# Kernel optimization log

Hardware: AMD Instinct MI355X
Metric: run time of the kernel (lower is better)

## Reference

```python
import jax, jax.numpy as jnp
import numpy as np


def _unfold(x, ks, pad):
    # torch nn.Unfold ordering: flattened channel dim is (c, kh, kw), output (b, c*ks*ks, h*w)
    b, c, h, w = x.shape
    if ks == 1:
        return x.reshape(b, c, h * w)
    xp = jnp.pad(x, ((0, 0), (0, 0), (pad, pad), (pad, pad)))
    patches = jnp.stack([xp[:, :, i:i + h, j:j + w] for i in range(ks) for j in range(ks)], axis=2)  # (b,c,ks*ks,h,w)
    return patches.reshape(b, c * ks * ks, h * w)


def _cg_conv(x, weight, ce_w, gd_w, gd2_w, ci_w, ks, pad, g=8):
    # Content-gated conv: SE-style dynamic kernel generation + unfold + batched matmul
    b, c, h, w = x.shape
    oc = weight.shape[0]
    # AdaptiveMaxPool2d((ks,ks)); h,w divisible by ks so bins are uniform
    gl = x.reshape(b, c, ks, h // ks, ks, w // ks).max(axis=(3, 5)).reshape(b, c, ks * ks)
    ce2 = jnp.einsum('bck,nk->bcn', gl, ce_w)                      # (b,c,num_lat)
    out = jnp.einsum('bcn,kn->bck', jax.nn.relu(ce2), gd_w)        # (b,c,ks*ks)
    # channel path: (b,c//g,g,num_lat) -> transpose -> Linear(g -> oc/(c//g))
    t = jax.nn.relu(jnp.transpose(ce2.reshape(b, c // g, g, -1), (0, 1, 3, 2)))
    ocp = jnp.transpose(jnp.einsum('bpng,og->bpno', t, ci_w), (0, 1, 3, 2)).reshape(b, oc, -1)
    ocp = jnp.einsum('bon,kn->bok', jax.nn.relu(ocp), gd2_w)       # (b,oc,ks*ks)
    dyn = jax.nn.sigmoid(out[:, None, :, :] + ocp[:, :, None, :])  # (b,oc,c,ks*ks)
    dyn = dyn * weight.reshape(1, oc, c, ks * ks)
    x_un = _unfold(x, ks, pad)                                     # (b, c*ks*ks, h*w)
    y = jnp.einsum('bok,bkl->bol', dyn.reshape(b, oc, c * ks * ks), x_un)
    return y.reshape(b, oc, h, w)


def setup_inputs() -> dict:
    key = jax.random.key(0)
    ks_ = jax.random.split(key, 12)
    b, c_in, c_hid, c_out, H, W = 4, 64, 256, 64, 96, 96
    s = 0.02
    inp = {
        'x': jax.random.normal(ks_[0], (b, c_in, H, W), jnp.float32),
        # fc1: 1x1, num_lat = 1, ci: 8 -> 256//(64//8)=32
        'fc1_weight': jax.random.normal(ks_[1], (c_hid, c_in, 1, 1), jnp.float32) * s,
        'fc1_ce': jax.random.normal(ks_[2], (1, 1), jnp.float32) * s,
        'fc1_gd': jax.random.normal(ks_[3], (1, 1), jnp.float32) * s,
        'fc1_gd2': jax.random.normal(ks_[4], (1, 1), jnp.float32) * s,
        'fc1_ci': jax.random.normal(ks_[5], (32, 8), jnp.float32) * s,
        # fc2: 3x3, num_lat = 5, ci: 8 -> 64//(256//8)=2
        'fc2_weight': jax.random.normal(ks_[6], (c_out, c_hid, 3, 3), jnp.float32) * s,
        'fc2_ce': jax.random.normal(ks_[7], (5, 9), jnp.float32) * s,
        'fc2_gd': jax.random.normal(ks_[8], (9, 5), jnp.float32) * s,
        'fc2_gd2': jax.random.normal(ks_[9], (9, 5), jnp.float32) * s,
        'fc2_ci': jax.random.normal(ks_[10], (2, 8), jnp.float32) * s,
    }
    return inp


def reference(x, fc1_weight, fc1_ce, fc1_gd, fc1_gd2, fc1_ci,
              fc2_weight, fc2_ce, fc2_gd, fc2_gd2, fc2_ci):
    h = _cg_conv(x, fc1_weight, fc1_ce, fc1_gd, fc1_gd2, fc1_ci, ks=1, pad=0)
    h = jax.nn.gelu(h, approximate=False)  # torch nn.GELU default is exact erf
    return _cg_conv(h, fc2_weight, fc2_ce, fc2_gd, fc2_gd2, fc2_ci, ks=3, pad=1)
```

## Files before the change

### kernel.cpp

```cpp
#include <hip/hip_runtime.h>
#include <math.h>

typedef __attribute__((ext_vector_type(8))) short short8x;
typedef __attribute__((ext_vector_type(4))) float float4x;
typedef unsigned short u16;
typedef unsigned int u32;

__device__ __forceinline__ float bf2f(u16 u) {
    return __uint_as_float(((u32)u) << 16);
}
__device__ __forceinline__ u16 f2bf(float f) {
    u32 u = __float_as_uint(f);
    u32 r = (u + 0x7fffu + ((u >> 16) & 1u)) >> 16;
    return (u16)r;
}
__device__ __forceinline__ u32 fenc(float f) {
    u32 b = __float_as_uint(f);
    return b ^ (0x80000000u | (u32)((int)b >> 31));
}
__device__ __forceinline__ float fdec(u32 u) {
    u32 b = (u & 0x80000000u) ? (u ^ 0x80000000u) : ~u;
    return __uint_as_float(b);
}


__global__ __launch_bounds__(256) void k_gl1(const float* __restrict__ x, float* __restrict__ gl1,
                                             u32* __restrict__ h2p32, u32* __restrict__ gl2u) {
    if (blockIdx.x >= 256) {
        int t = threadIdx.x;
        int plane_id = blockIdx.x - 256;
        u32* plane = h2p32 + plane_id * (98 * 98 * 16);
        for (int i = t; i < 1568; i += 256) plane[i] = 0u;
        for (int i = t; i < 1568; i += 256) plane[97 * 98 * 16 + i] = 0u;
        for (int i = t; i < 3072; i += 256) {
            int r = (i >> 5) + 1;
            int p = ((i >> 4) & 1) * 97;
            int w = i & 15;
            plane[(r * 98 + p) * 16 + w] = 0u;
        }
        for (int i = plane_id * 288 + t; i < (plane_id + 1) * 288; i += 256)
            gl2u[i] = 0u;
        return;
    }
    int b = blockIdx.x >> 6, c = blockIdx.x & 63;
    const float4* p = (const float4*)(x + (b * 64 + c) * 9216);
    float m = -1e30f;
    #pragma unroll
    for (int i = 0; i < 9; i++) {
        float4 v = p[i * 256 + threadIdx.x];
        m = fmaxf(m, fmaxf(fmaxf(v.x, v.y), fmaxf(v.z, v.w)));
    }
    __shared__ float red[256];
    red[threadIdx.x] = m;
    __syncthreads();
    for (int s = 128; s > 0; s >>= 1) {
        if (threadIdx.x < s) red[threadIdx.x] = fmaxf(red[threadIdx.x], red[threadIdx.x + s]);
        __syncthreads();
    }
    if (threadIdx.x == 0) gl1[b * 64 + c] = red[0];
}

__global__ __launch_bounds__(256) void k_gate1(const float* __restrict__ gl1,
                                               const float* __restrict__ ce, const float* __restrict__ gd,
                                               const float* __restrict__ gd2, const float* __restrict__ ci,
                                               const float* __restrict__ w1, u16* __restrict__ W1A) {
    int b = blockIdx.x >> 4, s = blockIdx.x & 15;
    int t = threadIdx.x;
    __shared__ float rce[64], out1[64], ocp[256];
    float cew = ce[0], gdw = gd[0], gd2w = gd2[0];
    if (t < 64) {
        float r = fmaxf(gl1[b * 64 + t] * cew, 0.f);
        rce[t] = r;
        out1[t] = r * gdw;
    }
    __syncthreads();
    {
        int p = t >> 5, oi = t & 31;
        float sv = 0.f;
        #pragma unroll
        for (int g = 0; g < 8; g++) sv += rce[p * 8 + g] * ci[oi * 8 + g];
        ocp[t] = fmaxf(sv, 0.f) * gd2w;
    }
    __syncthreads();
    u16* Wb = W1A + b * 256 * 64;
    #pragma unroll
    for (int i = 0; i < 4; i++) {
        int idx = s * 1024 + i * 256 + t;
        int o = idx >> 6, c = idx & 63;
        float v = out1[c] + ocp[o];
        float sg = 1.f / (1.f + expf(-v));
        Wb[idx] = f2bf(sg * w1[idx]);
    }
}

__global__ __launch_bounds__(256) void k_gemm1(const u16* __restrict__ W1A, const float* __restrict__ x,
                                               u16* __restrict__ h2p, u32* __restrict__ gl2u) {
    int bi = blockIdx.x;
    int b = bi / 192, rem = bi % 192;
    int y = rem >> 1, half = rem & 1;
    int t = threadIdx.x, wave = t >> 6, lane = t & 63, l15 = lane & 15, quad = lane >> 4;

    __shared__ __align__(16) u16 xs[48 * 72];
    const float* xb = x + (b * 64) * 9216 + y * 96 + half * 48;
    const float2* xb2 = (const float2*)xb;
    #pragma unroll
    for (int i = 0; i < 6; i++) {
        int idx = i * 256 + t;
        int c = idx / 24, px2 = idx - c * 24;
        float2 v = xb2[c * 4608 + px2];
        int px = px2 * 2;
        xs[px * 72 + c] = f2bf(v.x);
        xs[(px + 1) * 72 + c] = f2bf(v.y);
    }
    __syncthreads();

    float4x acc[4][3];
    #pragma unroll
    for (int mt = 0; mt < 4; mt++)
        #pragma unroll
        for (int nt = 0; nt < 3; nt++) acc[mt][nt] = (float4x){0.f, 0.f, 0.f, 0.f};
    const u16* Wb = W1A + b * 256 * 64;
    #pragma unroll
    for (int c0 = 0; c0 < 64; c0 += 32) {
        short8x bfr[3];
        #pragma unroll
        for (int nt = 0; nt < 3; nt++)
            bfr[nt] = *(const short8x*)(xs + (nt * 16 + l15) * 72 + c0 + quad * 8);
        #pragma unroll
        for (int mt = 0; mt < 4; mt++) {
            int oc = wave * 64 + mt * 16 + l15;
            short8x afr = *(const short8x*)(Wb + oc * 64 + c0 + quad * 8);
            #pragma unroll
            for (int nt = 0; nt < 3; nt++)
                acc[mt][nt] = __builtin_amdgcn_mfma_f32_16x16x32_bf16(afr, bfr[nt], acc[mt][nt], 0, 0, 0);
        }
    }
    const float is2 = 0.70710678118654752f;
    float gf[4][3][4];
    #pragma unroll
    for (int mt = 0; mt < 4; mt++) {
        #pragma unroll
        for (int nt = 0; nt < 3; nt++) {
            int xx = half * 48 + nt * 16 + l15;
            int oc0 = wave * 64 + mt * 16 + quad * 4;
            int g = oc0 >> 5, cl = oc0 & 31;
            u16 pk[4];
            #pragma unroll
            for (int r = 0; r < 4; r++) {
                float v = acc[mt][nt][r];
                float gl = 0.5f * v * (1.f + erff(v * is2));
                gf[mt][nt][r] = gl;
                pk[r] = f2bf(gl);
            }
            u16* dst = h2p + ((((b * 8 + g) * 98 + y + 1) * 98) + xx + 1) * 32 + cl;
            *(ushort4*)dst = make_ushort4(pk[0], pk[1], pk[2], pk[3]);
        }
    }
    int ki = y >> 5;
    int kA = ki * 3 + (half == 0 ? 0 : 1);
    int kB = ki * 3 + (half == 0 ? 1 : 2);
    #pragma unroll
    for (int mt = 0; mt < 4; mt++) {
        float vA[4], vB[4];
        #pragma unroll
        for (int r = 0; r < 4; r++) {
            if (half == 0) { vA[r] = fmaxf(gf[mt][0][r], gf[mt][1][r]); vB[r] = gf[mt][2][r]; }
            else           { vA[r] = gf[mt][0][r]; vB[r] = fmaxf(gf[mt][1][r], gf[mt][2][r]); }
        }
        #pragma unroll
        for (int m = 1; m < 16; m <<= 1) {
            #pragma unroll
            for (int r = 0; r < 4; r++) {
                vA[r] = fmaxf(vA[r], __shfl_xor(vA[r], m));
                vB[r] = fmaxf(vB[r], __shfl_xor(vB[r], m));
            }
        }
        if (l15 == 0) {
            #pragma unroll
            for (int r = 0; r < 4; r++) {
                int oc = wave * 64 + mt * 16 + quad * 4 + r;
                atomicMax(&gl2u[(b * 9 + kA) * 256 + oc], fenc(vA[r]));
                atomicMax(&gl2u[(b * 9 + kB) * 256 + oc], fenc(vB[r]));
            }
        }
    }
}

__global__ __launch_bounds__(256) void k_gate2(const u32* __restrict__ gl2u,
                                               const float* __restrict__ ce, const float* __restrict__ gd,
                                               const float* __restrict__ gd2, const float* __restrict__ ci,
                                               const float* __restrict__ w2, u16* __restrict__ W2A) {
    int b = blockIdx.x >> 4, s = blockIdx.x & 15;
    int t = threadIdx.x;
    __shared__ float rce[256][5];
    __shared__ float out2[256][9];
    __shared__ float ocp2[64][9];
    {
        float gl[9];
        #pragma unroll
        for (int k = 0; k < 9; k++) gl[k] = fdec(gl2u[(b * 9 + k) * 256 + t]);
        float r[5];
        #pragma unroll
        for (int n = 0; n < 5; n++) {
            float sv = 0.f;
            #pragma unroll
            for (int k = 0; k < 9; k++) sv += gl[k] * ce[n * 9 + k];
            r[n] = fmaxf(sv, 0.f);
            rce[t][n] = r[n];
        }
        #pragma unroll
        for (int k = 0; k < 9; k++) {
            float sv = 0.f;
            #pragma unroll
            for (int n = 0; n < 5; n++) sv += r[n] * gd[k * 5 + n];
            out2[t][k] = sv;
        }
    }
    __syncthreads();
    if (t < 64) {
        int p = t >> 1, oi = t & 1;
        float rt[5];
        #pragma unroll
        for (int n = 0; n < 5; n++) {
            float sv = 0.f;
            #pragma unroll
            for (int g = 0; g < 8; g++) sv += rce[p * 8 + g][n] * ci[oi * 8 + g];
            rt[n] = fmaxf(sv, 0.f);
        }
        #pragma unroll
        for (int k = 0; k < 9; k++) {
            float sv = 0.f;
            #pragma unroll
            for (int n = 0; n < 5; n++) sv += rt[n] * gd2[k * 5 + n];
            ocp2[t][k] = sv;
        }
    }
    __syncthreads();
    u16* Wb = W2A + b * (8 * 9 * 64 * 32);
    for (int it = 0; it < 36; it++) {
        int flat = s * 9216 + it * 256 + t;
        int cl = flat & 31;
        int o = (flat >> 5) & 63;
        int rest = flat >> 11;
        int k = rest % 9, g = rest / 9;
        int c = g * 32 + cl;
        float v = out2[c][k] + ocp2[o][k];
        float sg = 1.f / (1.f + expf(-v));
        Wb[flat] = f2bf(sg * w2[(o * 256 + c) * 9 + k]);
    }
}

__global__ __launch_bounds__(256) void k_conv2(const u16* __restrict__ W2A, const u16* __restrict__ h2p,
                                               float* __restrict__ out) {
    int bi = blockIdx.x;
    int b = bi / 192, rem = bi % 192;
    int y = rem >> 1, half = rem & 1;
    int t = threadIdx.x, wave = t >> 6, lane = t & 63, l15 = lane & 15, quad = lane >> 4;
    __shared__ __align__(16) u16 Bls[2][3 * 50 * 32];

    int offs[3];
    #pragma unroll
    for (int j = 0; j < 3; j++) {
        int i = t + j * 256;
        int r = i / 200, c16 = i - r * 200;
        offs[j] = ((y + r) * 98 + half * 48) * 32 + c16 * 8;
    }
    const int plane_sz = 98 * 98 * 32;
    uint4 p0, p1, p2;
    {
        const u16* pl = h2p + (b * 8) * plane_sz;
        p0 = *(const uint4*)(pl + offs[0]);
        p1 = *(const uint4*)(pl + offs[1]);
        if (t < 88) p2 = *(const uint4*)(pl + offs[2]);
        uint4* Bd = (uint4*)Bls[0];
        Bd[t] = p0;
        Bd[t + 256] = p1;
        if (t < 88) Bd[t + 512] = p2;
    }

    float4x acc[3];
    #pragma unroll
    for (int nt = 0; nt < 3; nt++) acc[nt] = (float4x){0.f, 0.f, 0.f, 0.f};

    for (int g = 0; g < 8; g++) {
        __syncthreads();
        if (g < 7) {
            const u16* pl = h2p + (b * 8 + g + 1) * plane_sz;
            p0 = *(const uint4*)(pl + offs[0]);
            p1 = *(const uint4*)(pl + offs[1]);
            if (t < 88) p2 = *(const uint4*)(pl + offs[2]);
        }
        const u16* Wg = W2A + (b * 8 + g) * (9 * 64 * 32);
        const u16* Bcur = Bls[g & 1];
        #pragma unroll
        for (int k = 0; k < 9; k++) {
            int ki = k / 3, kj = k - ki * 3;
            short8x af = *(const short8x*)(Wg + (k * 64 + wave * 16 + l15) * 32 + quad * 8);
            #pragma unroll
            for (int nt = 0; nt < 3; nt++) {
                int pxl = nt * 16 + l15 + kj;
                short8x bf = *(const short8x*)(Bcur + (ki * 50 + pxl) * 32 + quad * 8);
                acc[nt] = __builtin_amdgcn_mfma_f32_16x16x32_bf16(af, bf, acc[nt], 0, 0, 0);
            }
        }
        if (g < 7) {
            uint4* Bd = (uint4*)Bls[(g + 1) & 1];
            Bd[t] = p0;
            Bd[t + 256] = p1;
            if (t < 88) Bd[t + 512] = p2;
        }
    }
    #pragma unroll
    for (int nt = 0; nt < 3; nt++) {
        int xx = half * 48 + nt * 16 + l15;
        #pragma unroll
        for (int r = 0; r < 4; r++) {
            int oc = wave * 16 + quad * 4 + r;
            out[((b * 64 + oc) * 96 + y) * 96 + xx] = acc[nt][r];
        }
    }
}

extern "C" void kernel_launch(void* const* d_in, const int* in_sizes, int n_in,
                              void* d_out, int out_size, void* d_ws, size_t ws_size,
                              hipStream_t stream) {
    const float* x    = (const float*)d_in[0];
    const float* w1   = (const float*)d_in[1];
    const float* ce1  = (const float*)d_in[2];
    const float* gd1  = (const float*)d_in[3];
    const float* gd21 = (const float*)d_in[4];
    const float* ci1  = (const float*)d_in[5];
    const float* w2   = (const float*)d_in[6];
    const float* ce2  = (const float*)d_in[7];
    const float* gd2  = (const float*)d_in[8];
    const float* gd22 = (const float*)d_in[9];
    const float* ci2  = (const float*)d_in[10];
    float* out = (float*)d_out;

    char* ws = (char*)d_ws;
    u16*   h2p  = (u16*)(ws + 4718592);
    u16*   W1A  = (u16*)(ws + 24387584);
    u16*   W2A  = (u16*)(ws + 24518656);
    float* gl1  = (float*)(ws + 25698304);
    u32*   gl2u = (u32*)(ws + 25796608);

    k_gl1  <<<288, 256, 0, stream>>>(x, gl1, (u32*)h2p, gl2u);
    k_gate1<<<64,  256, 0, stream>>>(gl1, ce1, gd1, gd21, ci1, w1, W1A);
    k_gemm1<<<768, 256, 0, stream>>>(W1A, x, h2p, gl2u);
    k_gate2<<<64,  256, 0, stream>>>(gl2u, ce2, gd2, gd22, ci2, w2, W2A);
    k_conv2<<<768, 256, 0, stream>>>(W2A, h2p, out);
}
```

Before: 132.9 us.

## Split conv2 channel-group reduction across two wave groups with LDS reduce

The conv2 kernel now launches 512 threads per block. Two groups of four waves each process half of the eight channel groups, each with its own double-buffered LDS tile. Their partial accumulators are then summed through shared memory before the store. The intent is to shorten the serial K-loop and add in-block parallelism to hide latency. The cost is extra LDS, an extra reduction pass with barriers, and possibly lower block occupancy.

```diff
diff --git a/kernel.cpp b/kernel.cpp
--- a/kernel.cpp
+++ b/kernel.cpp
@@ -250,52 +250,61 @@
     }
 }
 
-__global__ __launch_bounds__(256) void k_conv2(const u16* __restrict__ W2A, const u16* __restrict__ h2p,
+__global__ __launch_bounds__(512) void k_conv2(const u16* __restrict__ W2A, const u16* __restrict__ h2p,
                                                float* __restrict__ out) {
     int bi = blockIdx.x;
     int b = bi / 192, rem = bi % 192;
     int y = rem >> 1, half = rem & 1;
-    int t = threadIdx.x, wave = t >> 6, lane = t & 63, l15 = lane & 15, quad = lane >> 4;
-    __shared__ __align__(16) u16 Bls[2][3 * 50 * 32];
+    int t = threadIdx.x, w = t >> 6, lane = t & 63, l15 = lane & 15, quad = lane >> 4;
+    int gh = w >> 2;
+    int ow = w & 3;
+    int th = t & 255;
+
+    __shared__ __align__(16) char smem[38400];
+    u16* Bls = (u16*)smem;
+    float* red = (float*)smem;
 
     int offs[3];
     #pragma unroll
     for (int j = 0; j < 3; j++) {
-        int i = t + j * 256;
+        int i = th + j * 256;
         int r = i / 200, c16 = i - r * 200;
         offs[j] = ((y + r) * 98 + half * 48) * 32 + c16 * 8;
     }
     const int plane_sz = 98 * 98 * 32;
+    const u16* plbase = h2p + (b * 8 + gh * 4) * plane_sz;
+
     uint4 p0, p1, p2;
     {
-        const u16* pl = h2p + (b * 8) * plane_sz;
+        const u16* pl = plbase;
         p0 = *(const uint4*)(pl + offs[0]);
         p1 = *(const uint4*)(pl + offs[1]);
-        if (t < 88) p2 = *(const uint4*)(pl + offs[2]);
-        uint4* Bd = (uint4*)Bls[0];
-        Bd[t] = p0;
-        Bd[t + 256] = p1;
-        if (t < 88) Bd[t + 512] = p2;
+        if (th < 88) p2 = *(const uint4*)(pl + offs[2]);
+        uint4* Bd = (uint4*)(Bls + gh * 2 * 4800);
+        Bd[th] = p0;
+        Bd[th + 256] = p1;
+        if (th < 88) Bd[th + 512] = p2;
     }
 
     float4x acc[3];
     #pragma unroll
     for (int nt = 0; nt < 3; nt++) acc[nt] = (float4x){0.f, 0.f, 0.f, 0.f};
 
-    for (int g = 0; g < 8; g++) {
+    for (int s = 0; s < 4; s++) {
         __syncthreads();
-        if (g < 7) {
-            const u16* pl = h2p + (b * 8 + g + 1) * plane_sz;
+        if (s < 3) {
+            const u16* pl = plbase + (s + 1) * plane_sz;
             p0 = *(const uint4*)(pl + offs[0]);
             p1 = *(const uint4*)(pl + offs[1]);
-            if (t < 88) p2 = *(const uint4*)(pl + offs[2]);
-        }
+            if (th < 88) p2 = *(const uint4*)(pl + offs[2]);
+        }
+        int g = gh * 4 + s;
         const u16* Wg = W2A + (b * 8 + g) * (9 * 64 * 32);
-        const u16* Bcur = Bls[g & 1];
+        const u16* Bcur = Bls + (gh * 2 + (s & 1)) * 4800;
         #pragma unroll
         for (int k = 0; k < 9; k++) {
             int ki = k / 3, kj = k - ki * 3;
-            short8x af = *(const short8x*)(Wg + (k * 64 + wave * 16 + l15) * 32 + quad * 8);
+            short8x af = *(const short8x*)(Wg + (k * 64 + ow * 16 + l15) * 32 + quad * 8);
             #pragma unroll
             for (int nt = 0; nt < 3; nt++) {
                 int pxl = nt * 16 + l15 + kj;
@@ -303,20 +312,33 @@
                 acc[nt] = __builtin_amdgcn_mfma_f32_16x16x32_bf16(af, bf, acc[nt], 0, 0, 0);
             }
         }
-        if (g < 7) {
-            uint4* Bd = (uint4*)Bls[(g + 1) & 1];
-            Bd[t] = p0;
-            Bd[t + 256] = p1;
-            if (t < 88) Bd[t + 512] = p2;
-        }
-    }
-    #pragma unroll
-    for (int nt = 0; nt < 3; nt++) {
-        int xx = half * 48 + nt * 16 + l15;
-        #pragma unroll
-        for (int r = 0; r < 4; r++) {
-            int oc = wave * 16 + quad * 4 + r;
-            out[((b * 64 + oc) * 96 + y) * 96 + xx] = acc[nt][r];
+        if (s < 3) {
+            uint4* Bd = (uint4*)(Bls + (gh * 2 + ((s + 1) & 1)) * 4800);
+            Bd[th] = p0;
+            Bd[th + 256] = p1;
+            if (th < 88) Bd[th + 512] = p2;
+        }
+    }
+
+    __syncthreads();
+    if (gh == 1) {
+        #pragma unroll
+        for (int nt = 0; nt < 3; nt++)
+            #pragma unroll
+            for (int r = 0; r < 4; r++)
+                red[(ow * 64 + lane) * 13 + nt * 4 + r] = acc[nt][r];
+    }
+    __syncthreads();
+    if (gh == 0) {
+        #pragma unroll
+        for (int nt = 0; nt < 3; nt++) {
+            int xx = half * 48 + nt * 16 + l15;
+            #pragma unroll
+            for (int r = 0; r < 4; r++) {
+                int oc = ow * 16 + quad * 4 + r;
+                float v = acc[nt][r] + red[(ow * 64 + lane) * 13 + nt * 4 + r];
+                out[((b * 64 + oc) * 96 + y) * 96 + xx] = v;
+            }
         }
     }
 }
@@ -348,5 +370,5 @@
     k_gate1<<<64,  256, 0, stream>>>(gl1, ce1, gd1, gd21, ci1, w1, W1A);
     k_gemm1<<<768, 256, 0, stream>>>(W1A, x, h2p, gl2u);
     k_gate2<<<64,  256, 0, stream>>>(gl2u, ce2, gd2, gd22, ci2, w2, W2A);
-    k_conv2<<<768, 256, 0, stream>>>(W2A, h2p, out);
-}
+    k_conv2<<<768, 512, 0, stream>>>(W2A, h2p, out);
+}
```

Measured after the change: 137.0 us. +3.1%, slower.
